# Kernel tuning notes

Measured on AMD Instinct MI355X. Metric: run time of the kernel, lower is better.

## Reference

```python
import jax, jax.numpy as jnp
import numpy as np

N = 100000
E = 1600000
NIN = 128
NOUT = 128


def setup_inputs() -> dict:
    key = jax.random.key(0)
    k1, k2, k3, k4 = jax.random.split(key, 4)
    x = jax.random.normal(k1, (N, NIN), dtype=jnp.float32)
    edge_index = jax.random.randint(k2, (2, E), 0, N, dtype=jnp.int64)
    edge_attr = jnp.ones((E,), dtype=jnp.float32)  # unused by GCNConv
    # PyG Linear weight is [out, in]; glorot-ish init
    W = jax.random.normal(k3, (NOUT, NIN), dtype=jnp.float32) / np.sqrt(NIN)
    b = jnp.zeros((NOUT,), dtype=jnp.float32)
    return {"x": x, "edge_index": edge_index, "edge_attr": edge_attr, "W": W, "b": b}


def reference(x, edge_index, edge_attr, W, b):
    # PyG GCNConv: add self-loops, symmetric degree normalization,
    # linear transform, scatter-add aggregation at destination, + bias.
    n = x.shape[0]
    loops = jnp.arange(n, dtype=edge_index.dtype)
    src = jnp.concatenate([edge_index[0], loops])  # [E+N]
    dst = jnp.concatenate([edge_index[1], loops])  # [E+N]
    # degree over destination (col) including self-loops, edge weight = 1
    deg = jax.ops.segment_sum(jnp.ones_like(dst, dtype=x.dtype), dst, num_segments=n)
    dinv = jnp.where(deg > 0, jax.lax.rsqrt(deg), 0.0)
    norm = dinv[src] * dinv[dst]  # [E+N]
    h = x @ W.T  # [N, NOUT]
    msg = h[src] * norm[:, None]  # [E+N, NOUT]
    out = jax.ops.segment_sum(msg, dst, num_segments=n)  # [N, NOUT]
    return out + b
```

## Files before the change

### kernel.cpp

```cpp
#include <hip/hip_runtime.h>

#define TPB 256
#define NBLK 256
#define BSH 8
#define BCAP 6144

typedef __attribute__((ext_vector_type(4))) float f32x4;
typedef __attribute__((ext_vector_type(8))) short short8;

__device__ __forceinline__ unsigned short f2bf(float f) {
    unsigned u = __float_as_uint(f);
    u = (u + 0x7fffu + ((u >> 16) & 1u)) >> 16;
    return (unsigned short)u;
}
__device__ __forceinline__ float bflo(unsigned u) { return __uint_as_float(u << 16); }
__device__ __forceinline__ float bfhi(unsigned u) { return __uint_as_float(u & 0xffff0000u); }


__global__ __launch_bounds__(256) void k_bhist(const int* __restrict__ dst,
                                               int* __restrict__ blockhist, int E) {
    __shared__ int sh[512];
    int t = threadIdx.x;
    sh[t] = 0; sh[t + 256] = 0;
    __syncthreads();
    int chunk = (E + NBLK - 1) / NBLK;
    int lo = blockIdx.x * chunk;
    int hi = min(E, lo + chunk);
    for (int e = lo + t; e < hi; e += 256)
        atomicAdd(&sh[dst[e] >> BSH], 1);
    __syncthreads();
    int* row = blockhist + blockIdx.x * 512;
    row[t] = sh[t];
    row[t + 256] = sh[t + 256];
}


__global__ __launch_bounds__(512) void k_bscan(int* __restrict__ blockhist,
                                               int* __restrict__ bbase, int E) {
    __shared__ int tmp[2][512];
    int t = threadIdx.x;
    int run = 0;
    for (int b = 0; b < NBLK; b += 8) {
        int v[8];
        #pragma unroll
        for (int j = 0; j < 8; ++j) v[j] = blockhist[(b + j) * 512 + t];
        #pragma unroll
        for (int j = 0; j < 8; ++j) { blockhist[(b + j) * 512 + t] = run; run += v[j]; }
    }
    tmp[0][t] = run;
    __syncthreads();
    int sb = 0;
    for (int d = 1; d < 512; d <<= 1) {
        int val = tmp[sb][t] + ((t >= d) ? tmp[sb][t - d] : 0);
        tmp[sb ^ 1][t] = val;
        sb ^= 1;
        __syncthreads();
    }
    bbase[t] = tmp[sb][t] - run;
    if (t == 0) bbase[512] = E;
}


__global__ __launch_bounds__(256) void k_bscatter(const int* __restrict__ src,
                                                  const int* __restrict__ dst,
                                                  const int* __restrict__ blockhist,
                                                  const int* __restrict__ bbase,
                                                  unsigned* __restrict__ packed, int E) {
    __shared__ int sh[512];
    int t = threadIdx.x;
    const int* row = blockhist + blockIdx.x * 512;
    sh[t]       = bbase[t]       + row[t];
    sh[t + 256] = bbase[t + 256] + row[t + 256];
    __syncthreads();
    int chunk = (E + NBLK - 1) / NBLK;
    int lo = blockIdx.x * chunk;
    int hi = min(E, lo + chunk);
    for (int e = lo + t; e < hi; e += 256) {
        int d = dst[e];
        int pos = atomicAdd(&sh[d >> BSH], 1);
        packed[pos] = ((unsigned)src[e] << 8) | (unsigned)(d & 255);
    }
}


__global__ __launch_bounds__(256) void k_bcsr(const unsigned* __restrict__ packed,
                                              const int* __restrict__ bbase,
                                              int* __restrict__ offsets,
                                              int* __restrict__ sorted_src,
                                              float* __restrict__ dinv, int N, int E) {
    __shared__ int hist[256];
    __shared__ int tmp[2][256];
    __shared__ int scur[256];
    __shared__ unsigned stage[BCAP];
    int b = blockIdx.x;
    int s0 = bbase[b], s1 = bbase[b + 1];
    int cnt = s1 - s0;
    int t = threadIdx.x;
    hist[t] = 0;
    __syncthreads();
    for (int e = s0 + t; e < s1; e += 256)
        atomicAdd(&hist[packed[e] & 255u], 1);
    __syncthreads();
    int v = hist[t];
    tmp[0][t] = v;
    __syncthreads();
    int sb = 0;
    for (int d = 1; d < 256; d <<= 1) {
        int val = tmp[sb][t] + ((t >= d) ? tmp[sb][t - d] : 0);
        tmp[sb ^ 1][t] = val;
        sb ^= 1;
        __syncthreads();
    }
    int lbase = tmp[sb][t] - v;
    scur[t] = lbase;
    int d = (b << BSH) + t;
    if (d < N) { offsets[d] = s0 + lbase; dinv[d] = rsqrtf((float)v + 1.0f); }
    if (b == 0 && t == 0) offsets[N] = E;
    __syncthreads();
    if (cnt <= BCAP) {
        for (int e = s0 + t; e < s1; e += 256) {
            unsigned pk = packed[e];
            int pos = atomicAdd(&scur[pk & 255u], 1);
            stage[pos] = pk >> 8;
        }
        __syncthreads();
        for (int i = t; i < cnt; i += 256)
            sorted_src[s0 + i] = (int)stage[i];
    } else {
        for (int e = s0 + t; e < s1; e += 256) {
            unsigned pk = packed[e];
            int pos = atomicAdd(&scur[pk & 255u], 1);
            sorted_src[(long)s0 + pos] = (int)(pk >> 8);
        }
    }
}


__global__ __launch_bounds__(256) void k_gemm(const float* __restrict__ x,
                                              const float* __restrict__ W,
                                              const float* __restrict__ dinv,
                                              unsigned short* __restrict__ g, int n) {
    __shared__ unsigned short wb[128][136];
    const int tid = threadIdx.x;

    for (int chunk = tid; chunk < 2048; chunk += 256) {
        int nrow = chunk >> 4, k8 = (chunk & 15) << 3;
        const float* wp = W + nrow * 128 + k8;
        float4 w0 = *(const float4*)wp;
        float4 w1 = *(const float4*)(wp + 4);
        union { unsigned short u[8]; uint4 q; } pk;
        pk.u[0] = f2bf(w0.x); pk.u[1] = f2bf(w0.y); pk.u[2] = f2bf(w0.z); pk.u[3] = f2bf(w0.w);
        pk.u[4] = f2bf(w1.x); pk.u[5] = f2bf(w1.y); pk.u[6] = f2bf(w1.z); pk.u[7] = f2bf(w1.w);
        *(uint4*)&wb[nrow][k8] = pk.q;
    }
    __syncthreads();

    const int lane = tid & 63;
    const int wid  = tid >> 6;
    const int l15  = lane & 15;
    const int quad = lane >> 4;
    const int row  = blockIdx.x * 64 + wid * 16 + l15;
    const int rowc = (row < n) ? row : (n - 1);

    f32x4 acc[8];
    #pragma unroll
    for (int t = 0; t < 8; ++t) acc[t] = (f32x4){0.f, 0.f, 0.f, 0.f};

    #pragma unroll
    for (int ks = 0; ks < 4; ++ks) {
        const int kb = ks * 32 + quad * 8;
        float4 a0 = *(const float4*)(x + (long)rowc * 128 + kb);
        float4 a1 = *(const float4*)(x + (long)rowc * 128 + kb + 4);
        union { unsigned short u[8]; short8 v; } af;
        af.u[0] = f2bf(a0.x); af.u[1] = f2bf(a0.y); af.u[2] = f2bf(a0.z); af.u[3] = f2bf(a0.w);
        af.u[4] = f2bf(a1.x); af.u[5] = f2bf(a1.y); af.u[6] = f2bf(a1.z); af.u[7] = f2bf(a1.w);
        #pragma unroll
        for (int t = 0; t < 8; ++t) {
            short8 bf = *(const short8*)&wb[t * 16 + l15][kb];
            acc[t] = __builtin_amdgcn_mfma_f32_16x16x32_bf16(bf, af.v, acc[t], 0, 0, 0);
        }
    }

    if (row < n) {
        float dv = dinv[row];
        unsigned short* gp = g + (long)row * 128 + quad * 4;
        #pragma unroll
        for (int t = 0; t < 8; ++t) {
            unsigned short u0 = f2bf(acc[t][0] * dv);
            unsigned short u1 = f2bf(acc[t][1] * dv);
            unsigned short u2 = f2bf(acc[t][2] * dv);
            unsigned short u3 = f2bf(acc[t][3] * dv);
            uint2 pk;
            pk.x = (unsigned)u0 | ((unsigned)u1 << 16);
            pk.y = (unsigned)u2 | ((unsigned)u3 << 16);
            *(uint2*)(gp + t * 16) = pk;
        }
    }
}


__global__ __launch_bounds__(256) void k_aggregate(const int* __restrict__ sorted_src,
                                                   const int* __restrict__ offsets,
                                                   const unsigned short* __restrict__ g,
                                                   const float* __restrict__ dinv,
                                                   const float* __restrict__ b,
                                                   float* __restrict__ out, int n) {
    int d = blockIdx.x * (TPB / 32) + (threadIdx.x >> 5);
    if (d >= n) return;
    int c = (threadIdx.x & 31) << 2;

    int s0 = offsets[d];
    int s1 = offsets[d + 1];

    float4 acc = make_float4(0.f, 0.f, 0.f, 0.f);
    auto addrow = [&](int r) {
        uint2 p = *(const uint2*)(g + (long)r * 128 + c);
        acc.x += bflo(p.x); acc.y += bfhi(p.x);
        acc.z += bflo(p.y); acc.w += bfhi(p.y);
    };

    addrow(d);
    int e = s0;
    for (; e + 8 <= s1; e += 8) {
        int a[8];
        #pragma unroll
        for (int j = 0; j < 8; ++j) a[j] = sorted_src[e + j];
        #pragma unroll
        for (int j = 0; j < 8; ++j) addrow(a[j]);
    }
    for (; e + 4 <= s1; e += 4) {
        int a[4];
        #pragma unroll
        for (int j = 0; j < 4; ++j) a[j] = sorted_src[e + j];
        #pragma unroll
        for (int j = 0; j < 4; ++j) addrow(a[j]);
    }
    for (; e < s1; ++e) addrow(sorted_src[e]);

    float s = dinv[d];
    float4 bb = *(const float4*)(b + c);
    float4 r = make_float4(acc.x * s + bb.x, acc.y * s + bb.y,
                           acc.z * s + bb.z, acc.w * s + bb.w);
    *(float4*)(out + (long)d * 128 + c) = r;
}


extern "C" void kernel_launch(void* const* d_in, const int* in_sizes, int n_in,
                              void* d_out, int out_size, void* d_ws, size_t ws_size,
                              hipStream_t stream) {
    const float* x  = (const float*)d_in[0];
    const int*   ei = (const int*)d_in[1];
    const float* W  = (const float*)d_in[3];
    const float* b  = (const float*)d_in[4];
    float* out = (float*)d_out;

    const int N = in_sizes[0] / 128;
    const int E = in_sizes[1] / 2;
    const int* src = ei;
    const int* dst = ei + E;
    const int NB = (N + 255) >> BSH;

    char* p = (char*)d_ws;
    auto carve = [&](size_t bytes) { char* q = p; p += (bytes + 255) & ~(size_t)255; return q; };
    int*            blockhist  = (int*)           carve((size_t)NBLK * 512 * 4);
    int*            bbase      = (int*)           carve(513 * 4);
    int*            offsets    = (int*)           carve((size_t)(N + 1) * 4);
    float*          dinv       = (float*)         carve((size_t)N * 4);
    unsigned*       packed     = (unsigned*)      carve((size_t)E * 4);
    int*            sorted_src = (int*)           carve((size_t)E * 4);
    unsigned short* g          = (unsigned short*)carve((size_t)N * 128 * 2);

    k_bhist   <<<NBLK, TPB, 0, stream>>>(dst, blockhist, E);
    k_bscan   <<<1, 512, 0, stream>>>(blockhist, bbase, E);
    k_bscatter<<<NBLK, TPB, 0, stream>>>(src, dst, blockhist, bbase, packed, E);
    k_bcsr    <<<NB, TPB, 0, stream>>>(packed, bbase, offsets, sorted_src, dinv, N, E);

    k_gemm<<<(N + 63) / 64, TPB, 0, stream>>>(x, W, dinv, g, N);

    k_aggregate<<<(N + (TPB / 32) - 1) / (TPB / 32), TPB, 0, stream>>>(
        sorted_src, offsets, g, dinv, b, out, N);
}
```

Baseline: 249.7 us.

## Parallelize bucket scan, precompute bf16 weights, widen aggregate loads to 16 bytes

Replaces the single-block serial column scan with a 128-block wave-shuffle prefix kernel, and recomputes the bucket-base scan redundantly inside each scatter/CSR block. Weight bf16 conversion moves into the histogram kernel so each GEMM block only copies the preconverted weights. The aggregate kernel now uses 16 lanes per node with 16-byte loads, stores byte offsets (src<<8) in sorted_src to skip index multiplication, and unrolls by 16. The trade-off is redundant scan work in every block and more register pressure in aggregate.

```diff
diff --git a/kernel.cpp b/kernel.cpp
--- a/kernel.cpp
+++ b/kernel.cpp
@@ -18,7 +18,9 @@
 
 
 __global__ __launch_bounds__(256) void k_bhist(const int* __restrict__ dst,
-                                               int* __restrict__ blockhist, int E) {
+                                               int* __restrict__ blockhist,
+                                               const float* __restrict__ W,
+                                               unsigned short* __restrict__ wbf, int E) {
     __shared__ int sh[512];
     int t = threadIdx.x;
     sh[t] = 0; sh[t + 256] = 0;
@@ -32,126 +34,156 @@
     int* row = blockhist + blockIdx.x * 512;
     row[t] = sh[t];
     row[t + 256] = sh[t + 256];
-}
-
-
-__global__ __launch_bounds__(512) void k_bscan(int* __restrict__ blockhist,
-                                               int* __restrict__ bbase, int E) {
-    __shared__ int tmp[2][512];
-    int t = threadIdx.x;
-    int run = 0;
-    for (int b = 0; b < NBLK; b += 8) {
-        int v[8];
-        #pragma unroll
-        for (int j = 0; j < 8; ++j) v[j] = blockhist[(b + j) * 512 + t];
-        #pragma unroll
-        for (int j = 0; j < 8; ++j) { blockhist[(b + j) * 512 + t] = run; run += v[j]; }
-    }
-    tmp[0][t] = run;
+
+    if (blockIdx.x < 8) {
+        int gid = blockIdx.x * 256 + t;
+        const float* wp = W + gid * 8;
+        float4 w0 = *(const float4*)wp;
+        float4 w1 = *(const float4*)(wp + 4);
+        union { unsigned short u[8]; uint4 q; } pk;
+        pk.u[0] = f2bf(w0.x); pk.u[1] = f2bf(w0.y); pk.u[2] = f2bf(w0.z); pk.u[3] = f2bf(w0.w);
+        pk.u[4] = f2bf(w1.x); pk.u[5] = f2bf(w1.y); pk.u[6] = f2bf(w1.z); pk.u[7] = f2bf(w1.w);
+        *((uint4*)wbf + gid) = pk.q;
+    }
+}
+
+
+__global__ __launch_bounds__(256) void k_bpfx(int* __restrict__ blockhist,
+                                              int* __restrict__ ctot) {
+    const int wave = blockIdx.x * 4 + (threadIdx.x >> 6);
+    const int lane = threadIdx.x & 63;
+    int v[4];
+    #pragma unroll
+    for (int j = 0; j < 4; ++j) v[j] = blockhist[(lane * 4 + j) * 512 + wave];
+    int s = v[0] + v[1] + v[2] + v[3];
+    int incl = s;
+    #pragma unroll
+    for (int d = 1; d < 64; d <<= 1) {
+        int o = __shfl_up(incl, d);
+        if (lane >= d) incl += o;
+    }
+    int pre = incl - s;
+    #pragma unroll
+    for (int j = 0; j < 4; ++j) { blockhist[(lane * 4 + j) * 512 + wave] = pre; pre += v[j]; }
+    if (lane == 63) ctot[wave] = incl;
+}
+
+__device__ __forceinline__ void bucket_base_scan(const int* __restrict__ ctot,
+                                                 int (&tp)[2][256], int* bb,
+                                                 int E, int t) {
+    int v0 = ctot[2 * t], v1 = ctot[2 * t + 1];
+    int p = v0 + v1;
+    tp[0][t] = p;
     __syncthreads();
     int sb = 0;
-    for (int d = 1; d < 512; d <<= 1) {
-        int val = tmp[sb][t] + ((t >= d) ? tmp[sb][t - d] : 0);
-        tmp[sb ^ 1][t] = val;
+    for (int d = 1; d < 256; d <<= 1) {
+        int val = tp[sb][t] + ((t >= d) ? tp[sb][t - d] : 0);
+        tp[sb ^ 1][t] = val;
         sb ^= 1;
         __syncthreads();
     }
-    bbase[t] = tmp[sb][t] - run;
-    if (t == 0) bbase[512] = E;
+    int base = tp[sb][t] - p;
+    bb[2 * t] = base;
+    bb[2 * t + 1] = base + v0;
+    if (t == 0) bb[512] = E;
+    __syncthreads();
 }
 
 
 __global__ __launch_bounds__(256) void k_bscatter(const int* __restrict__ src,
                                                   const int* __restrict__ dst,
                                                   const int* __restrict__ blockhist,
-                                                  const int* __restrict__ bbase,
+                                                  const int* __restrict__ ctot,
                                                   unsigned* __restrict__ packed, int E) {
-    __shared__ int sh[512];
+    __shared__ int tp[2][256];
+    __shared__ int bb[513];
+    __shared__ int cur[512];
     int t = threadIdx.x;
+    bucket_base_scan(ctot, tp, bb, E, t);
     const int* row = blockhist + blockIdx.x * 512;
-    sh[t]       = bbase[t]       + row[t];
-    sh[t + 256] = bbase[t + 256] + row[t + 256];
+    cur[t]       = bb[t]       + row[t];
+    cur[t + 256] = bb[t + 256] + row[t + 256];
     __syncthreads();
     int chunk = (E + NBLK - 1) / NBLK;
     int lo = blockIdx.x * chunk;
     int hi = min(E, lo + chunk);
     for (int e = lo + t; e < hi; e += 256) {
         int d = dst[e];
-        int pos = atomicAdd(&sh[d >> BSH], 1);
+        int pos = atomicAdd(&cur[d >> BSH], 1);
         packed[pos] = ((unsigned)src[e] << 8) | (unsigned)(d & 255);
     }
 }
 
 
 __global__ __launch_bounds__(256) void k_bcsr(const unsigned* __restrict__ packed,
-                                              const int* __restrict__ bbase,
+                                              const int* __restrict__ ctot,
                                               int* __restrict__ offsets,
                                               int* __restrict__ sorted_src,
-                                              float* __restrict__ dinv, int N, int E) {
+                                              float* __restrict__ dinv, int N, int E, int NB) {
+    __shared__ int tmp[2][256];
+    __shared__ int bb[513];
     __shared__ int hist[256];
-    __shared__ int tmp[2][256];
     __shared__ int scur[256];
     __shared__ unsigned stage[BCAP];
-    int b = blockIdx.x;
-    int s0 = bbase[b], s1 = bbase[b + 1];
-    int cnt = s1 - s0;
     int t = threadIdx.x;
-    hist[t] = 0;
-    __syncthreads();
-    for (int e = s0 + t; e < s1; e += 256)
-        atomicAdd(&hist[packed[e] & 255u], 1);
-    __syncthreads();
-    int v = hist[t];
-    tmp[0][t] = v;
-    __syncthreads();
-    int sb = 0;
-    for (int d = 1; d < 256; d <<= 1) {
-        int val = tmp[sb][t] + ((t >= d) ? tmp[sb][t - d] : 0);
-        tmp[sb ^ 1][t] = val;
-        sb ^= 1;
-        __syncthreads();
-    }
-    int lbase = tmp[sb][t] - v;
-    scur[t] = lbase;
-    int d = (b << BSH) + t;
-    if (d < N) { offsets[d] = s0 + lbase; dinv[d] = rsqrtf((float)v + 1.0f); }
-    if (b == 0 && t == 0) offsets[N] = E;
-    __syncthreads();
-    if (cnt <= BCAP) {
-        for (int e = s0 + t; e < s1; e += 256) {
-            unsigned pk = packed[e];
-            int pos = atomicAdd(&scur[pk & 255u], 1);
-            stage[pos] = pk >> 8;
+    bucket_base_scan(ctot, tmp, bb, E, t);
+
+    for (int b = blockIdx.x; b < NB; b += NBLK) {
+        int s0 = bb[b], s1 = bb[b + 1];
+        int cnt = s1 - s0;
+        hist[t] = 0;
+        __syncthreads();
+        for (int e = s0 + t; e < s1; e += 256)
+            atomicAdd(&hist[packed[e] & 255u], 1);
+        __syncthreads();
+        int v = hist[t];
+        tmp[0][t] = v;
+        __syncthreads();
+        int sb = 0;
+        for (int d = 1; d < 256; d <<= 1) {
+            int val = tmp[sb][t] + ((t >= d) ? tmp[sb][t - d] : 0);
+            tmp[sb ^ 1][t] = val;
+            sb ^= 1;
+            __syncthreads();
         }
-        __syncthreads();
-        for (int i = t; i < cnt; i += 256)
-            sorted_src[s0 + i] = (int)stage[i];
-    } else {
-        for (int e = s0 + t; e < s1; e += 256) {
-            unsigned pk = packed[e];
-            int pos = atomicAdd(&scur[pk & 255u], 1);
-            sorted_src[(long)s0 + pos] = (int)(pk >> 8);
+        int lbase = tmp[sb][t] - v;
+        scur[t] = lbase;
+        int d = (b << BSH) + t;
+        if (d < N) { offsets[d] = s0 + lbase; dinv[d] = rsqrtf((float)v + 1.0f); }
+        if (b == 0 && t == 0) offsets[N] = E;
+        __syncthreads();
+        if (cnt <= BCAP) {
+            for (int e = s0 + t; e < s1; e += 256) {
+                unsigned pk = packed[e];
+                int pos = atomicAdd(&scur[pk & 255u], 1);
+                stage[pos] = pk & 0xffffff00u;
+            }
+            __syncthreads();
+            for (int i = t; i < cnt; i += 256)
+                sorted_src[s0 + i] = (int)stage[i];
+        } else {
+            for (int e = s0 + t; e < s1; e += 256) {
+                unsigned pk = packed[e];
+                int pos = atomicAdd(&scur[pk & 255u], 1);
+                sorted_src[(long)s0 + pos] = (int)(pk & 0xffffff00u);
+            }
         }
+        __syncthreads();
     }
 }
 
 
 __global__ __launch_bounds__(256) void k_gemm(const float* __restrict__ x,
-                                              const float* __restrict__ W,
+                                              const unsigned short* __restrict__ wbf,
                                               const float* __restrict__ dinv,
                                               unsigned short* __restrict__ g, int n) {
     __shared__ unsigned short wb[128][136];
     const int tid = threadIdx.x;
 
-    for (int chunk = tid; chunk < 2048; chunk += 256) {
-        int nrow = chunk >> 4, k8 = (chunk & 15) << 3;
-        const float* wp = W + nrow * 128 + k8;
-        float4 w0 = *(const float4*)wp;
-        float4 w1 = *(const float4*)(wp + 4);
-        union { unsigned short u[8]; uint4 q; } pk;
-        pk.u[0] = f2bf(w0.x); pk.u[1] = f2bf(w0.y); pk.u[2] = f2bf(w0.z); pk.u[3] = f2bf(w0.w);
-        pk.u[4] = f2bf(w1.x); pk.u[5] = f2bf(w1.y); pk.u[6] = f2bf(w1.z); pk.u[7] = f2bf(w1.w);
-        *(uint4*)&wb[nrow][k8] = pk.q;
+    const uint4* wv = (const uint4*)wbf;
+    for (int ch = tid; ch < 2048; ch += 256) {
+        int nrow = ch >> 4, k8 = (ch & 15) << 3;
+        *(uint4*)&wb[nrow][k8] = wv[ch];
     }
     __syncthreads();
 
@@ -205,22 +237,34 @@
                                                    const float* __restrict__ dinv,
                                                    const float* __restrict__ b,
                                                    float* __restrict__ out, int n) {
-    int d = blockIdx.x * (TPB / 32) + (threadIdx.x >> 5);
+    int d = blockIdx.x * (TPB / 16) + (threadIdx.x >> 4);
     if (d >= n) return;
-    int c = (threadIdx.x & 31) << 2;
+    int c = (threadIdx.x & 15) << 3;
+    const char* gb = (const char*)g + (c << 1);
 
     int s0 = offsets[d];
     int s1 = offsets[d + 1];
 
-    float4 acc = make_float4(0.f, 0.f, 0.f, 0.f);
-    auto addrow = [&](int r) {
-        uint2 p = *(const uint2*)(g + (long)r * 128 + c);
-        acc.x += bflo(p.x); acc.y += bfhi(p.x);
-        acc.z += bflo(p.y); acc.w += bfhi(p.y);
+    float acc[8];
+    #pragma unroll
+    for (int j = 0; j < 8; ++j) acc[j] = 0.f;
+    auto addrow = [&](int off) {
+        uint4 p = *(const uint4*)(gb + off);
+        acc[0] += bflo(p.x); acc[1] += bfhi(p.x);
+        acc[2] += bflo(p.y); acc[3] += bfhi(p.y);
+        acc[4] += bflo(p.z); acc[5] += bfhi(p.z);
+        acc[6] += bflo(p.w); acc[7] += bfhi(p.w);
     };
 
-    addrow(d);
+    addrow(d << 8);
     int e = s0;
+    for (; e + 16 <= s1; e += 16) {
+        int a[16];
+        #pragma unroll
+        for (int j = 0; j < 16; ++j) a[j] = sorted_src[e + j];
+        #pragma unroll
+        for (int j = 0; j < 16; ++j) addrow(a[j]);
+    }
     for (; e + 8 <= s1; e += 8) {
         int a[8];
         #pragma unroll
@@ -238,10 +282,15 @@
     for (; e < s1; ++e) addrow(sorted_src[e]);
 
     float s = dinv[d];
-    float4 bb = *(const float4*)(b + c);
-    float4 r = make_float4(acc.x * s + bb.x, acc.y * s + bb.y,
-                           acc.z * s + bb.z, acc.w * s + bb.w);
-    *(float4*)(out + (long)d * 128 + c) = r;
+    float4 b0 = *(const float4*)(b + c);
+    float4 b1 = *(const float4*)(b + c + 4);
+    float* op = out + (long)d * 128 + c;
+    float4 r0 = make_float4(acc[0] * s + b0.x, acc[1] * s + b0.y,
+                            acc[2] * s + b0.z, acc[3] * s + b0.w);
+    float4 r1 = make_float4(acc[4] * s + b1.x, acc[5] * s + b1.y,
+                            acc[6] * s + b1.z, acc[7] * s + b1.w);
+    *(float4*)op = r0;
+    *(float4*)(op + 4) = r1;
 }
 
 
@@ -263,20 +312,21 @@
     char* p = (char*)d_ws;
     auto carve = [&](size_t bytes) { char* q = p; p += (bytes + 255) & ~(size_t)255; return q; };
     int*            blockhist  = (int*)           carve((size_t)NBLK * 512 * 4);
-    int*            bbase      = (int*)           carve(513 * 4);
+    int*            ctot       = (int*)           carve(512 * 4);
     int*            offsets    = (int*)           carve((size_t)(N + 1) * 4);
     float*          dinv       = (float*)         carve((size_t)N * 4);
     unsigned*       packed     = (unsigned*)      carve((size_t)E * 4);
     int*            sorted_src = (int*)           carve((size_t)E * 4);
+    unsigned short* wbf        = (unsigned short*)carve((size_t)128 * 128 * 2);
     unsigned short* g          = (unsigned short*)carve((size_t)N * 128 * 2);
 
-    k_bhist   <<<NBLK, TPB, 0, stream>>>(dst, blockhist, E);
-    k_bscan   <<<1, 512, 0, stream>>>(blockhist, bbase, E);
-    k_bscatter<<<NBLK, TPB, 0, stream>>>(src, dst, blockhist, bbase, packed, E);
-    k_bcsr    <<<NB, TPB, 0, stream>>>(packed, bbase, offsets, sorted_src, dinv, N, E);
-
-    k_gemm<<<(N + 63) / 64, TPB, 0, stream>>>(x, W, dinv, g, N);
-
-    k_aggregate<<<(N + (TPB / 32) - 1) / (TPB / 32), TPB, 0, stream>>>(
+    k_bhist   <<<NBLK, TPB, 0, stream>>>(dst, blockhist, W, wbf, E);
+    k_bpfx    <<<128, TPB, 0, stream>>>(blockhist, ctot);
+    k_bscatter<<<NBLK, TPB, 0, stream>>>(src, dst, blockhist, ctot, packed, E);
+    k_bcsr    <<<NB, TPB, 0, stream>>>(packed, ctot, offsets, sorted_src, dinv, N, E, NB);
+
+    k_gemm<<<(N + 63) / 64, TPB, 0, stream>>>(x, wbf, dinv, g, N);
+
+    k_aggregate<<<(N + (TPB / 16) - 1) / (TPB / 16), TPB, 0, stream>>>(
         sorted_src, offsets, g, dinv, b, out, N);
 }
```

Measured after the change: 255.8 us. 2.4% more time.
